# Kernel tuning notes

Hardware: AMD Instinct MI355X
Metric: run time of the kernel (lower is better)

Reference implementation:

```python
import jax, jax.numpy as jnp
import numpy as np

FP4_E2M1_VALUES = [0.0, 0.0625, 8.0, 1.0, 2.0, 3.0, 4.0, 6.0,
                   -0.0, -0.0625, -8.0, -1.0, -2.0, -3.0, -4.0, -6.0]

M, N, K = 4096, 4096, 4096


def setup_inputs() -> dict:
    key = jax.random.key(0)
    k1, k2 = jax.random.split(key)
    x = jax.random.normal(k1, (M, K), dtype=jnp.float16)
    # packed uint8 bytes stored as int32 (values in [0,256)); each byte holds
    # two fp4 indices: high nibble = even k, low nibble = odd k
    packed_weight = jax.random.randint(k2, (N, K // 2), 0, 256, dtype=jnp.int32)
    lut = jnp.array(FP4_E2M1_VALUES, dtype=jnp.float16)
    return {"x": x, "packed_weight": packed_weight, "lut": lut}


def reference(x, packed_weight, lut):
    # Dequantize: unpack nibbles along K, LUT lookup -> W [N, K] fp16
    n, kh = packed_weight.shape
    high = (packed_weight >> 4) & 15   # even k positions
    low = packed_weight & 15           # odd k positions
    idx = jnp.stack([high, low], axis=-1).reshape(n, 2 * kh)  # [N, K]
    w = lut[idx]                       # [N, K] fp16
    # GEMM with fp32 accumulation (Triton kernel accumulates in fp32), cast to fp16
    y = jnp.einsum('mk,nk->mn', x, w, preferred_element_type=jnp.float32)
    return y.astype(jnp.float16)
```

## Files before the change

### kernel.cpp

```cpp
#include <hip/hip_runtime.h>
#include <hip/hip_fp16.h>
#include <stdint.h>

#define M_DIM 4096
#define N_DIM 4096
#define K_DIM 4096
#define BM 128
#define BN 128
#define BK 32
#define KW (K_DIM / 2)

typedef _Float16 half8 __attribute__((ext_vector_type(8)));
typedef float f32x4 __attribute__((ext_vector_type(4)));

__device__ __forceinline__ uint32_t pk2(float a, float b) {
  auto h = __builtin_amdgcn_cvt_pkrtz(a, b);
  return __builtin_bit_cast(uint32_t, h);
}

__device__ __forceinline__ uint32_t dq(uint32_t b, uint32_t ph, uint32_t pl) {
#if __has_builtin(__builtin_amdgcn_perm)
  const uint32_t sel = ((b & 0x70u) << 4) | ((b & 0x07u) << 24);
  uint32_t v = __builtin_amdgcn_perm(ph, pl, sel);
#else
  const uint64_t pool = ((uint64_t)ph << 32) | pl;
  const uint32_t mh = (uint32_t)(pool >> (((b >> 4) & 7u) * 8)) & 0xFFu;
  const uint32_t ml = (uint32_t)(pool >> ((b & 7u) * 8)) & 0xFFu;
  uint32_t v = (mh << 8) | (ml << 24);
#endif
  const uint32_t sg = ((b & 0x88u) * 0x10000100u) & 0x80008000u;
  return v | sg;
}

__global__ __launch_bounds__(256) void cvt_x_kernel(const float4* __restrict__ xin,
                                                    uint4* __restrict__ xout) {
  const int i = blockIdx.x * 256 + threadIdx.x;
  const float4 v0 = xin[2 * i];
  const float4 v1 = xin[2 * i + 1];
  xout[i] = make_uint4(pk2(v0.x, v0.y), pk2(v0.z, v0.w),
                       pk2(v1.x, v1.y), pk2(v1.z, v1.w));
}

__global__ __launch_bounds__(256, 2) void fp4gemm_kernel(
    const uint8_t* __restrict__ xh,
    const int* __restrict__ pw,
    const float* __restrict__ lutf,
    float* __restrict__ out)
{
  __shared__ uint16_t ldsA[BM * BK];
  __shared__ uint16_t ldsB[BN * BK];

  const int tid  = threadIdx.x;
  const int lane = tid & 63;
  const int wave = tid >> 6;
  const int wm   = wave >> 1;
  const int wn   = wave & 1;
  const int m0 = blockIdx.y * BM;
  const int n0 = blockIdx.x * BN;

  const uint32_t h01 = pk2(lutf[0], lutf[1]);
  const uint32_t h23 = pk2(lutf[2], lutf[3]);
  const uint32_t h45 = pk2(lutf[4], lutf[5]);
  const uint32_t h67 = pk2(lutf[6], lutf[7]);
#if __has_builtin(__builtin_amdgcn_perm)
  const uint32_t pl = __builtin_amdgcn_perm(h23, h01, 0x07050301u);
  const uint32_t ph = __builtin_amdgcn_perm(h67, h45, 0x07050301u);
#else
  const uint32_t pl = ((h01 >> 8) & 0xFFu) | ((h01 >> 24) << 8) |
                      (((h23 >> 8) & 0xFFu) << 16) | ((h23 >> 24) << 24);
  const uint32_t ph = ((h45 >> 8) & 0xFFu) | ((h45 >> 24) << 8) |
                      (((h67 >> 8) & 0xFFu) << 16) | ((h67 >> 24) << 24);
#endif

  f32x4 acc[4][4];
#pragma unroll
  for (int i = 0; i < 4; ++i)
#pragma unroll
    for (int j = 0; j < 4; ++j) acc[i][j] = (f32x4){0.f, 0.f, 0.f, 0.f};

  const int rowB  = tid >> 1;
  const int halfB = tid & 1;
  const int swzB  = (rowB >> 1) & 3;

  for (int kt = 0; kt < K_DIM / BK; ++kt) {
    __syncthreads();

#pragma unroll
    for (int s = 0; s < 2; ++s) {
      const int idx = tid + s * 256;
      const int row = idx >> 2;
      const int c16 = idx & 3;
      const int g16 = c16 ^ ((row >> 1) & 3);
      const uint8_t* gp = xh + ((size_t)(m0 + row) * K_DIM + kt * BK) * 2 + g16 * 16;
      uint8_t* lp = (uint8_t*)ldsA + (size_t)idx * 16;
      __builtin_amdgcn_global_load_lds(
          (const __attribute__((address_space(1))) uint32_t*)gp,
          (__attribute__((address_space(3))) uint32_t*)lp, 16, 0, 0);
    }

    {
      const int* gp = pw + (size_t)(n0 + rowB) * KW + kt * (BK / 2) + halfB * 8;
      const int4 wA = ((const int4*)gp)[0];
      const int4 wB = ((const int4*)gp)[1];
      uint8_t* base = (uint8_t*)ldsB + rowB * 64;
      *(uint4*)(base + ((halfB * 2 + 0) ^ swzB) * 16) =
          make_uint4(dq(wA.x, ph, pl), dq(wA.y, ph, pl),
                     dq(wA.z, ph, pl), dq(wA.w, ph, pl));
      *(uint4*)(base + ((halfB * 2 + 1) ^ swzB) * 16) =
          make_uint4(dq(wB.x, ph, pl), dq(wB.y, ph, pl),
                     dq(wB.z, ph, pl), dq(wB.w, ph, pl));
    }

    __syncthreads();

    const int q = lane >> 4;
    half8 af[4], bfr[4];
#pragma unroll
    for (int i = 0; i < 4; ++i) {
      const int row = wm * 64 + i * 16 + (lane & 15);
      const uint16_t* pa = ldsA + row * BK + (q ^ ((row >> 1) & 3)) * 8;
      af[i] = *(const half8*)pa;
    }
#pragma unroll
    for (int j = 0; j < 4; ++j) {
      const int row = wn * 64 + j * 16 + (lane & 15);
      const uint16_t* pb = ldsB + row * BK + (q ^ ((row >> 1) & 3)) * 8;
      bfr[j] = *(const half8*)pb;
    }
#pragma unroll
    for (int i = 0; i < 4; ++i)
#pragma unroll
      for (int j = 0; j < 4; ++j)
        acc[i][j] = __builtin_amdgcn_mfma_f32_16x16x32_f16(af[i], bfr[j], acc[i][j], 0, 0, 0);
  }

  const int mb = m0 + wm * 64 + (lane >> 4) * 4;
  const int nb = n0 + wn * 64 + (lane & 15);
#pragma unroll
  for (int i = 0; i < 4; ++i)
#pragma unroll
    for (int j = 0; j < 4; ++j)
#pragma unroll
      for (int r = 0; r < 4; ++r)
        out[(size_t)(mb + i * 16 + r) * N_DIM + (nb + j * 16)] = acc[i][j][r];
}

extern "C" void kernel_launch(void* const* d_in, const int* in_sizes, int n_in,
                              void* d_out, int out_size, void* d_ws, size_t ws_size,
                              hipStream_t stream) {
  const void* px = nullptr; const void* ppw = nullptr; const void* plut = nullptr;
  for (int i = 0; i < n_in; ++i) {
    const long s = in_sizes[i];
    if (s == (long)M_DIM * K_DIM) px = d_in[i];
    else if (s == (long)N_DIM * KW) ppw = d_in[i];
    else if (s == 16) plut = d_in[i];
  }
  if (!px || !ppw || !plut) { px = d_in[0]; ppw = d_in[1]; plut = d_in[2]; }

  dim3 grid(N_DIM / BN, M_DIM / BM);

  cvt_x_kernel<<<(M_DIM * K_DIM / 8) / 256, 256, 0, stream>>>(
      (const float4*)px, (uint4*)d_ws);
  fp4gemm_kernel<<<grid, dim3(256), 0, stream>>>(
      (const uint8_t*)d_ws, (const int*)ppw, (const float*)plut, (float*)d_out);
}
```

Before: 298.2 us.

## Split weight dequantization into a prepass and use pure fp16 GEMM

Adds a separate kernel that dequantizes the packed fp4 weights into a full fp16 matrix in workspace. The GEMM then streams both operands straight into LDS with global_load_lds, instead of having every block redo register-side dequant and LDS stores on each K tile. This removes dequant work that was repeated across the M-blocks, at the cost of an extra pass that writes and rereads a 32 MB fp16 weight matrix. It falls back to the fused kernel when the workspace is too small.

```diff
diff --git a/kernel.cpp b/kernel.cpp
--- a/kernel.cpp
+++ b/kernel.cpp
@@ -9,6 +9,8 @@
 #define BN 128
 #define BK 32
 #define KW (K_DIM / 2)
+#define WS_XH_BYTES ((size_t)M_DIM * K_DIM * 2)
+#define WS_WH_BYTES ((size_t)N_DIM * K_DIM * 2)
 
 typedef _Float16 half8 __attribute__((ext_vector_type(8)));
 typedef float f32x4 __attribute__((ext_vector_type(4)));
@@ -32,6 +34,23 @@
   return v | sg;
 }
 
+__device__ __forceinline__ void lut_pool(const float* __restrict__ lutf,
+                                         uint32_t& ph, uint32_t& pl) {
+  const uint32_t h01 = pk2(lutf[0], lutf[1]);
+  const uint32_t h23 = pk2(lutf[2], lutf[3]);
+  const uint32_t h45 = pk2(lutf[4], lutf[5]);
+  const uint32_t h67 = pk2(lutf[6], lutf[7]);
+#if __has_builtin(__builtin_amdgcn_perm)
+  pl = __builtin_amdgcn_perm(h23, h01, 0x07050301u);
+  ph = __builtin_amdgcn_perm(h67, h45, 0x07050301u);
+#else
+  pl = ((h01 >> 8) & 0xFFu) | ((h01 >> 24) << 8) |
+       (((h23 >> 8) & 0xFFu) << 16) | ((h23 >> 24) << 24);
+  ph = ((h45 >> 8) & 0xFFu) | ((h45 >> 24) << 8) |
+       (((h67 >> 8) & 0xFFu) << 16) | ((h67 >> 24) << 24);
+#endif
+}
+
 __global__ __launch_bounds__(256) void cvt_x_kernel(const float4* __restrict__ xin,
                                                     uint4* __restrict__ xout) {
   const int i = blockIdx.x * 256 + threadIdx.x;
@@ -39,6 +58,96 @@
   const float4 v1 = xin[2 * i + 1];
   xout[i] = make_uint4(pk2(v0.x, v0.y), pk2(v0.z, v0.w),
                        pk2(v1.x, v1.y), pk2(v1.z, v1.w));
+}
+
+__global__ __launch_bounds__(256) void wdq_kernel(const int4* __restrict__ pin,
+                                                  uint4* __restrict__ wout,
+                                                  const float* __restrict__ lutf) {
+  uint32_t ph, pl;
+  lut_pool(lutf, ph, pl);
+  const int i = blockIdx.x * 256 + threadIdx.x;
+  const int4 w = pin[i];
+  wout[i] = make_uint4(dq(w.x, ph, pl), dq(w.y, ph, pl),
+                       dq(w.z, ph, pl), dq(w.w, ph, pl));
+}
+
+__global__ __launch_bounds__(256, 2) void f16gemm_kernel(
+    const uint8_t* __restrict__ xh,
+    const uint8_t* __restrict__ wh,
+    float* __restrict__ out)
+{
+  __shared__ uint16_t ldsA[BM * BK];
+  __shared__ uint16_t ldsB[BN * BK];
+
+  const int tid  = threadIdx.x;
+  const int lane = tid & 63;
+  const int wave = tid >> 6;
+  const int wm   = wave >> 1;
+  const int wn   = wave & 1;
+  const int m0 = blockIdx.y * BM;
+  const int n0 = blockIdx.x * BN;
+
+  f32x4 acc[4][4];
+#pragma unroll
+  for (int i = 0; i < 4; ++i)
+#pragma unroll
+    for (int j = 0; j < 4; ++j) acc[i][j] = (f32x4){0.f, 0.f, 0.f, 0.f};
+
+  const uint8_t* xbase = xh + (size_t)m0 * K_DIM * 2;
+  const uint8_t* wbase = wh + (size_t)n0 * K_DIM * 2;
+
+  for (int kt = 0; kt < K_DIM / BK; ++kt) {
+    __syncthreads();
+
+#pragma unroll
+    for (int s = 0; s < 2; ++s) {
+      const int idx = tid + s * 256;
+      const int row = idx >> 2;
+      const int c16 = idx & 3;
+      const int g16 = c16 ^ ((row >> 1) & 3);
+      const size_t goff = ((size_t)row * K_DIM + kt * BK) * 2 + g16 * 16;
+      __builtin_amdgcn_global_load_lds(
+          (const __attribute__((address_space(1))) uint32_t*)(xbase + goff),
+          (__attribute__((address_space(3))) uint32_t*)((uint8_t*)ldsA + (size_t)idx * 16),
+          16, 0, 0);
+      __builtin_amdgcn_global_load_lds(
+          (const __attribute__((address_space(1))) uint32_t*)(wbase + goff),
+          (__attribute__((address_space(3))) uint32_t*)((uint8_t*)ldsB + (size_t)idx * 16),
+          16, 0, 0);
+    }
+
+    __syncthreads();
+
+    const int q = lane >> 4;
+    half8 af[4], bfr[4];
+#pragma unroll
+    for (int i = 0; i < 4; ++i) {
+      const int row = wm * 64 + i * 16 + (lane & 15);
+      const uint16_t* pa = ldsA + row * BK + (q ^ ((row >> 1) & 3)) * 8;
+      af[i] = *(const half8*)pa;
+    }
+#pragma unroll
+    for (int j = 0; j < 4; ++j) {
+      const int row = wn * 64 + j * 16 + (lane & 15);
+      const uint16_t* pb = ldsB + row * BK + (q ^ ((row >> 1) & 3)) * 8;
+      bfr[j] = *(const half8*)pb;
+    }
+#pragma unroll
+    for (int i = 0; i < 4; ++i)
+#pragma unroll
+      for (int j = 0; j < 4; ++j)
+        acc[i][j] = __builtin_amdgcn_mfma_f32_16x16x32_f16(af[i], bfr[j], acc[i][j], 0, 0, 0);
+  }
+
+  const int mb = m0 + wm * 64 + (lane >> 4) * 4;
+  const int nb = n0 + wn * 64 + (lane & 15);
+#pragma unroll
+  for (int i = 0; i < 4; ++i)
+#pragma unroll
+    for (int j = 0; j < 4; ++j)
+#pragma unroll
+      for (int r = 0; r < 4; ++r)
+        out[(size_t)(mb + i * 16 + r) * N_DIM + (nb + j * 16)] = acc[i][j][r];
 }
 
 __global__ __launch_bounds__(256, 2) void fp4gemm_kernel(
@@ -58,19 +167,8 @@
   const int m0 = blockIdx.y * BM;
   const int n0 = blockIdx.x * BN;
 
-  const uint32_t h01 = pk2(lutf[0], lutf[1]);
-  const uint32_t h23 = pk2(lutf[2], lutf[3]);
-  const uint32_t h45 = pk2(lutf[4], lutf[5]);
-  const uint32_t h67 = pk2(lutf[6], lutf[7]);
-#if __has_builtin(__builtin_amdgcn_perm)
-  const uint32_t pl = __builtin_amdgcn_perm(h23, h01, 0x07050301u);
-  const uint32_t ph = __builtin_amdgcn_perm(h67, h45, 0x07050301u);
-#else
-  const uint32_t pl = ((h01 >> 8) & 0xFFu) | ((h01 >> 24) << 8) |
-                      (((h23 >> 8) & 0xFFu) << 16) | ((h23 >> 24) << 24);
-  const uint32_t ph = ((h45 >> 8) & 0xFFu) | ((h45 >> 24) << 8) |
-                      (((h67 >> 8) & 0xFFu) << 16) | ((h67 >> 24) << 24);
-#endif
+  uint32_t ph, pl;
+  lut_pool(lutf, ph, pl);
 
   f32x4 acc[4][4];
 #pragma unroll
@@ -161,6 +259,15 @@
 
   cvt_x_kernel<<<(M_DIM * K_DIM / 8) / 256, 256, 0, stream>>>(
       (const float4*)px, (uint4*)d_ws);
-  fp4gemm_kernel<<<grid, dim3(256), 0, stream>>>(
-      (const uint8_t*)d_ws, (const int*)ppw, (const float*)plut, (float*)d_out);
-}
+
+  if (ws_size >= WS_XH_BYTES + WS_WH_BYTES) {
+    uint8_t* wh = (uint8_t*)d_ws + WS_XH_BYTES;
+    wdq_kernel<<<(N_DIM * KW / 4) / 256, 256, 0, stream>>>(
+        (const int4*)ppw, (uint4*)wh, (const float*)plut);
+    f16gemm_kernel<<<grid, dim3(256), 0, stream>>>(
+        (const uint8_t*)d_ws, wh, (float*)d_out);
+  } else {
+    fp4gemm_kernel<<<grid, dim3(256), 0, stream>>>(
+        (const uint8_t*)d_ws, (const int*)ppw, (const float*)plut, (float*)d_out);
+  }
+}
```

Measured after the change: 295.8 us. About the same (-0.8%).
